# Performance work log

Hardware: AMD Instinct MI355X
Metric: run time of the kernel (lower is better)

## Reference

```python
import jax, jax.numpy as jnp
import numpy as np
from math import factorial, sqrt, pi

LMAX, NSH = 2, 9
F = 64
N_RBF = 20
N_INTER = 2
N_ATOMS = 1000
N_PAIRS = 10000
CUTOFF = 5.0

# ---------- Clebsch-Gordan coefficients for real spherical harmonics ----------

def _cg_complex(l1, m1, l2, m2, l3, m3):
    # <l1 m1 l2 m2 | l3 m3> via Racah formula
    if m3 != m1 + m2 or not (abs(l1 - l2) <= l3 <= l1 + l2):
        return 0.0
    f = factorial
    pre = sqrt((2 * l3 + 1) * f(l3 + l1 - l2) * f(l3 - l1 + l2) * f(l1 + l2 - l3) / f(l1 + l2 + l3 + 1))
    pre *= sqrt(f(l3 + m3) * f(l3 - m3) * f(l1 - m1) * f(l1 + m1) * f(l2 - m2) * f(l2 + m2))
    s = 0.0
    for k in range(l1 + l2 - l3 + 1):
        d = [k, l1 + l2 - l3 - k, l1 - m1 - k, l2 + m2 - k, l3 - l2 + m1 + k, l3 - l1 - m2 + k]
        if min(d) < 0:
            continue
        s += (-1) ** k / np.prod([float(f(t)) for t in d])
    return pre * s

def _sh_indices(lmax):
    l = np.concatenate([np.full(2 * ll + 1, ll) for ll in range(lmax + 1)])
    m = np.concatenate([np.arange(-ll, ll + 1) for ll in range(lmax + 1)])
    return l, m

def _real_cg(lmax):
    lidx, midx = _sh_indices(lmax)
    n = (lmax + 1) ** 2
    cgc = np.zeros((n, n, n))
    for a in range(n):
        for b in range(n):
            for c in range(n):
                cgc[a, b, c] = _cg_complex(lidx[a], midx[a], lidx[b], midx[b], lidx[c], midx[c])
    # complex -> real spherical harmonic change of basis (per degree l)
    U = np.zeros((n, n), dtype=np.complex128)
    for ll in range(lmax + 1):
        base = ll * ll + ll
        U[base, base] = 1.0
        for m in range(1, ll + 1):
            U[base + m, base - m] = 1 / sqrt(2)
            U[base + m, base + m] = (-1) ** m / sqrt(2)
            U[base - m, base - m] = 1j / sqrt(2)
            U[base - m, base + m] = -1j * (-1) ** m / sqrt(2)
    cgr = np.einsum('ijk,ai,bj,ck->abc', cgc.astype(np.complex128), U, U, U.conj())
    parity = (-1.0) ** lidx
    mask = (parity[:, None, None] * parity[None, :, None]) == parity[None, None, :]
    cgr = np.real(cgr) * mask
    cgr = np.transpose(cgr, (2, 0, 1))  # [s_out, s_in(x), s_filter(Y)]
    s1, s2, s3 = np.nonzero(np.abs(cgr) > 1e-9)
    return s1, s2, s3, cgr[s1, s2, s3].astype(np.float32), lidx

_S1, _S2, _S3, _CGV, _LIDX = _real_cg(LMAX)
IDX1 = jnp.asarray(_S1)            # output sh channel per CG path
IDX2 = jnp.asarray(_S2)            # input-feature sh channel per CG path
IDX3 = jnp.asarray(_S3)            # Ylm sh channel per CG path
CGVAL = jnp.asarray(_CGV)          # CG value per path
WIDX = jnp.asarray(_LIDX[_S3])     # radial-filter degree per CG path
LIDX = jnp.asarray(_LIDX)          # degree of each of the 9 sh channels

# ---------- real spherical harmonics (lmax=2, orthonormal, m=-l..l order) ----------

def _rsh(u):
    x, y, z = u[:, 0], u[:, 1], u[:, 2]
    c1 = sqrt(3.0 / (4.0 * pi))
    c2 = 0.5 * sqrt(15.0 / pi)
    return jnp.stack([
        jnp.full_like(x, 0.5 / sqrt(pi)),
        c1 * y, c1 * z, c1 * x,
        c2 * x * y,
        c2 * y * z,
        0.25 * sqrt(5.0 / pi) * (3.0 * z * z - 1.0),
        c2 * x * z,
        0.25 * sqrt(15.0 / pi) * (x * x - y * y),
    ], axis=1)


def setup_inputs() -> dict:
    key = jax.random.key(0)
    ks = jax.random.split(key, 10)
    atomic_numbers = jax.random.randint(ks[0], (N_ATOMS,), 0, 100)
    r_ij = 1.5 * jax.random.normal(ks[1], (N_PAIRS, 3), dtype=jnp.float32)
    idx_i = jnp.sort(jax.random.randint(ks[2], (N_PAIRS,), 0, N_ATOMS))
    idx_j = jax.random.randint(ks[3], (N_PAIRS,), 0, N_ATOMS)
    emb = jax.random.normal(ks[4], (100, F), dtype=jnp.float32)
    def s(k, sh, fan):
        return jax.random.normal(k, sh, dtype=jnp.float32) / float(np.sqrt(fan))
    Wf = s(ks[5], (N_INTER, N_RBF, (LMAX + 1) * F), N_RBF)
    bf = jnp.zeros((N_INTER, (LMAX + 1) * F), jnp.float32)
    W1 = s(ks[6], (N_INTER, F, F), F)
    W2 = s(ks[7], (N_INTER, F, F), F)
    W3 = s(ks[8], (N_INTER, F, F), F)
    Wg = s(ks[9], (N_INTER, F, (LMAX + 1) * F), F)
    bg = jnp.zeros((N_INTER, (LMAX + 1) * F), jnp.float32)
    return dict(atomic_numbers=atomic_numbers, r_ij=r_ij, idx_i=idx_i, idx_j=idx_j,
                emb=emb, Wf=Wf, bf=bf, W1=W1, W2=W2, W3=W3, Wg=Wg, bg=bg)


def reference(atomic_numbers, r_ij, idx_i, idx_j, emb, Wf, bf, W1, W2, W3, Wg, bg):
    n_atoms = atomic_numbers.shape[0]
    d = jnp.linalg.norm(r_ij, axis=1, keepdims=True)          # [P,1]
    Yij = _rsh(r_ij / d)                                       # [P,9]
    offsets = jnp.linspace(0.0, CUTOFF, N_RBF)                 # GaussianRBF
    width = CUTOFF / (N_RBF - 1)
    radial = jnp.exp((-0.5 / (width * width)) * (d - offsets) ** 2)   # [P,n_rbf]
    cut = 0.5 * (jnp.cos(d * (pi / CUTOFF)) + 1.0) * (d < CUTOFF)     # [P,1]
    # nuclear embedding + scalar2rsh (zero-pad l>0 channels)
    x = jnp.zeros((n_atoms, NSH, F), emb.dtype).at[:, 0, :].set(emb[atomic_numbers])
    for t in range(N_INTER):
        # SO3Convolution
        Wij = (radial @ Wf[t] + bf[t]).reshape(-1, LMAX + 1, F) * cut[:, :, None]  # [P,lmax+1,F]
        xj = x[idx_j]                                                              # [P,9,F]
        v = xj[:, IDX2] * Yij[:, IDX3, None] * Wij[:, WIDX] * CGVAL[None, :, None]  # [P,nnz,F]
        yij = jnp.zeros_like(xj).at[:, IDX1].add(v)                                 # CG scatter
        dx = jax.ops.segment_sum(yij, idx_i, num_segments=n_atoms)                  # edge->node scatter
        # mixing1 + SO3TensorProduct
        ddx = dx @ W1[t]
        tp = jnp.zeros_like(dx).at[:, IDX1].add(dx[:, IDX2] * ddx[:, IDX3] * CGVAL[None, :, None])
        dx = (dx + tp) @ W2[t]
        # SO3ParametricGatedNonlinearity (gate from l=0 channel)
        gate = (dx[:, 0] @ Wg[t] + bg[t]).reshape(-1, LMAX + 1, F)
        dx = dx * jax.nn.sigmoid(gate[:, LIDX])
        dx = dx @ W3[t]
        x = x + dx
    return x  # multipole_representation [n_atoms, 9, F]; x[:,0] is scalar_representation
```

## Files before the change

### kernel.cpp

```cpp
#include <hip/hip_runtime.h>
#include <cmath>

constexpr int kNsh    = 9;
constexpr int kF      = 64;
constexpr int kNrbf   = 20;
constexpr int kNAtoms = 1000;
constexpr int kNPairs = 10000;
constexpr float kCutoffF = 5.0f;
constexpr int kMaxNZ  = 200;
constexpr int kCp     = 12;
constexpr int kXs     = kF * kCp;
constexpr int kChunk  = 32;
constexpr int kPdS    = 36;

struct CGSparse {
  int n;
  int c[kMaxNZ];
  int a[kMaxNZ];
  int b[kMaxNZ];
  float v[kMaxNZ];
};

constexpr double cfact(int n) {
  double r = 1.0;
  for (int i = 2; i <= n; i++) r *= (double)i;
  return r;
}
constexpr double cabs_(double x) { return x < 0 ? -x : x; }
constexpr double csqrt_(double x) {
  if (x <= 0.0) return 0.0;
  double g = x < 1.0 ? 1.0 : x;
  for (int i = 0; i < 60; i++) g = 0.5 * (g + x / g);
  return g;
}

constexpr double cg_cplx(int l1, int m1, int l2, int m2, int l3, int m3) {
  if (m3 != m1 + m2) return 0.0;
  int lo = l1 > l2 ? l1 - l2 : l2 - l1;
  if (l3 < lo || l3 > l1 + l2) return 0.0;
  double pre = csqrt_((2 * l3 + 1) * cfact(l3 + l1 - l2) * cfact(l3 - l1 + l2) *
                      cfact(l1 + l2 - l3) / cfact(l1 + l2 + l3 + 1));
  pre *= csqrt_(cfact(l3 + m3) * cfact(l3 - m3) * cfact(l1 - m1) *
                cfact(l1 + m1) * cfact(l2 - m2) * cfact(l2 + m2));
  double s = 0.0;
  for (int k = 0; k <= l1 + l2 - l3; k++) {
    int d0 = k, d1 = l1 + l2 - l3 - k, d2 = l1 - m1 - k;
    int d3 = l2 + m2 - k, d4 = l3 - l2 + m1 + k, d5 = l3 - l1 - m2 + k;
    if (d0 < 0 || d1 < 0 || d2 < 0 || d3 < 0 || d4 < 0 || d5 < 0) continue;
    double den = cfact(d0) * cfact(d1) * cfact(d2) * cfact(d3) * cfact(d4) * cfact(d5);
    s += ((k % 2) ? -1.0 : 1.0) / den;
  }
  return pre * s;
}

constexpr CGSparse build_cg() {
  CGSparse out{};
  int lidx[9] = {0, 1, 1, 1, 2, 2, 2, 2, 2};
  int midx[9] = {0, -1, 0, 1, -2, -1, 0, 1, 2};
  double Ur[9][9] = {};
  double Ui[9][9] = {};
  for (int l = 0; l <= 2; l++) {
    int base = l * l + l;
    Ur[base][base] = 1.0;
    for (int m = 1; m <= l; m++) {
      double s2 = 1.0 / csqrt_(2.0);
      double sgn = (m % 2) ? -1.0 : 1.0;
      Ur[base + m][base - m] = s2;
      Ur[base + m][base + m] = sgn * s2;
      Ui[base - m][base - m] = s2;
      Ui[base - m][base + m] = -sgn * s2;
    }
  }
  double cgr[9][9][9] = {};
  for (int i = 0; i < 9; i++)
    for (int j = 0; j < 9; j++)
      for (int k = 0; k < 9; k++) {
        double cv = cg_cplx(lidx[i], midx[i], lidx[j], midx[j], lidx[k], midx[k]);
        if (cv == 0.0) continue;
        for (int a2 = 0; a2 < 9; a2++) {
          if (Ur[a2][i] == 0.0 && Ui[a2][i] == 0.0) continue;
          for (int b2 = 0; b2 < 9; b2++) {
            if (Ur[b2][j] == 0.0 && Ui[b2][j] == 0.0) continue;
            for (int c2 = 0; c2 < 9; c2++) {
              if (Ur[c2][k] == 0.0 && Ui[c2][k] == 0.0) continue;
              double ar = Ur[a2][i], ai = Ui[a2][i];
              double br = Ur[b2][j], bi = Ui[b2][j];
              double cr = Ur[c2][k], ci = -Ui[c2][k];
              double pr = ar * br - ai * bi;
              double pi = ar * bi + ai * br;
              double rr = pr * cr - pi * ci;
              cgr[c2][a2][b2] += rr * cv;
            }
          }
        }
      }
  int n = 0;
  for (int c2 = 0; c2 < 9; c2++)
    for (int a2 = 0; a2 < 9; a2++)
      for (int b2 = 0; b2 < 9; b2++) {
        bool mask = ((lidx[a2] + lidx[b2]) % 2) == (lidx[c2] % 2);
        double v = mask ? cgr[c2][a2][b2] : 0.0;
        if (cabs_(v) > 1e-9) {
          out.c[n] = c2;
          out.a[n] = a2;
          out.b[n] = b2;
          out.v[n] = (float)v;
          n++;
        }
      }
  out.n = n;
  return out;
}

constexpr CGSparse CG = build_cg();
static_assert(CG.n > 0 && CG.n <= kMaxNZ, "CG table size out of range");

__device__ __forceinline__ void mm_stream(const float* __restrict__ sDx,
                                          const float* __restrict__ W,
                                          int f, float* __restrict__ acc) {
  #pragma unroll
  for (int c = 0; c < 9; c++) acc[c] = 0.f;
  #pragma unroll 4
  for (int kq = 0; kq < 16; kq++) {
    float w0 = W[(4 * kq + 0) * kF + f];
    float w1 = W[(4 * kq + 1) * kF + f];
    float w2 = W[(4 * kq + 2) * kF + f];
    float w3 = W[(4 * kq + 3) * kF + f];
    #pragma unroll
    for (int c = 0; c < 9; c++) {
      float4 dv = *(const float4*)(sDx + c * kF + 4 * kq);
      acc[c] += dv.x * w0 + dv.y * w1 + dv.z * w2 + dv.w * w3;
    }
  }
}

template <int T>
__global__ __launch_bounds__(64) void k_so3(
    const float* __restrict__ rij, const int* __restrict__ idx_i,
    const int* __restrict__ idx_j, const int* __restrict__ Z,
    const float* __restrict__ emb, const float* __restrict__ Wft,
    const float* __restrict__ bft, const float* __restrict__ W1,
    const float* __restrict__ W2, const float* __restrict__ W3,
    const float* __restrict__ Wg, const float* __restrict__ bg,
    const float* __restrict__ x_in, float* __restrict__ x_out) {
  const int atom = blockIdx.x;
  const int f = threadIdx.x;

  __shared__ __align__(16) float pdLDS[kChunk * kPdS];
  __shared__ __align__(16) float dxLDS[kNsh * kF];
  __shared__ __align__(16) float rowLDS[kF];

  float w0r[kNrbf], w1r[kNrbf], w2r[kNrbf];
  #pragma unroll
  for (int k = 0; k < kNrbf; k++) {
    w0r[k] = Wft[k * 192 + f];
    w1r[k] = Wft[k * 192 + 64 + f];
    w2r[k] = Wft[k * 192 + 128 + f];
  }
  const float bf0 = bft[f], bf1 = bft[64 + f], bf2 = bft[128 + f];

  int lo = 0;
  {
    const int a = atom + (f & 1);
    int hi = kNPairs;
    while (lo < hi) {
      int mid = (lo + hi) >> 1;
      if (idx_i[mid] < a) lo = mid + 1; else hi = mid;
    }
  }
  const int s0 = __builtin_amdgcn_readlane(lo, 0);
  const int s1 = __builtin_amdgcn_readlane(lo, 1);

  float y[9];
  #pragma unroll
  for (int c = 0; c < 9; c++) y[c] = 0.f;

  for (int cb = s0; cb < s1; cb += kChunk) {
    const int cn = (s1 - cb < kChunk) ? (s1 - cb) : kChunk;
    for (int item = f; item < cn * 32; item += 64) {
      const int pp = item >> 5, slot = item & 31;
      const int p = cb + pp;
      float rx = rij[3 * p + 0], ry = rij[3 * p + 1], rz = rij[3 * p + 2];
      float d = sqrtf(rx * rx + ry * ry + rz * rz);
      float inv = 1.0f / d;
      float ux = rx * inv, uy = ry * inv, uz = rz * inv;
      const float c0 = 0.28209479177387814f;
      const float c1 = 0.4886025119029199f;
      const float c2 = 1.0925484305920792f;
      const float c3 = 0.31539156525252005f;
      const float c4 = 0.5462742152960396f;
      float cut = (d < kCutoffF) ? 0.5f * (cosf(d * (float)(M_PI / 5.0)) + 1.0f) : 0.0f;
      float val;
      if (slot < 9) {
        val =
            (slot == 0) ? c0 :
            (slot == 1) ? c1 * uy :
            (slot == 2) ? c1 * uz :
            (slot == 3) ? c1 * ux :
            (slot == 4) ? c2 * ux * uy :
            (slot == 5) ? c2 * uy * uz :
            (slot == 6) ? c3 * (3.0f * uz * uz - 1.0f) :
            (slot == 7) ? c2 * ux * uz :
                          c4 * (ux * ux - uy * uy);
      } else if (slot == 9) {
        val = cut;
      } else if (slot >= 12) {
        const float width = kCutoffF / (kNrbf - 1);
        const float coef = -0.5f / (width * width);
        float off = (kCutoffF * (slot - 12)) / (kNrbf - 1);
        float tt = d - off;
        val = expf(coef * tt * tt) * cut;
      } else {
        continue;
      }
      pdLDS[pp * kPdS + slot] = val;
    }
    __syncthreads();

    for (int pp = 0; pp < cn; pp++) {
      const int p = cb + pp;
      const int j = idx_j[p];
      const float* pd = pdLDS + pp * kPdS;
      const float cut = pd[9];
      float Wl0 = bf0 * cut, Wl1 = bf1 * cut, Wl2 = bf2 * cut;
      #pragma unroll
      for (int kq = 0; kq < 5; kq++) {
        float4 r4 = *(const float4*)(pd + 12 + 4 * kq);
        Wl0 += r4.x * w0r[4 * kq] + r4.y * w0r[4 * kq + 1] +
               r4.z * w0r[4 * kq + 2] + r4.w * w0r[4 * kq + 3];
        Wl1 += r4.x * w1r[4 * kq] + r4.y * w1r[4 * kq + 1] +
               r4.z * w1r[4 * kq + 2] + r4.w * w1r[4 * kq + 3];
        Wl2 += r4.x * w2r[4 * kq] + r4.y * w2r[4 * kq + 1] +
               r4.z * w2r[4 * kq + 2] + r4.w * w2r[4 * kq + 3];
      }
      float YW[9];
      YW[0] = pd[0] * Wl0;
      YW[1] = pd[1] * Wl1;
      YW[2] = pd[2] * Wl1;
      YW[3] = pd[3] * Wl1;
      #pragma unroll
      for (int b = 4; b < 9; b++) YW[b] = pd[b] * Wl2;
      if (T == 0) {
        float e = emb[Z[j] * kF + f];
        #pragma unroll
        for (int q = 0; q < CG.n; q++) {
          if (CG.a[q] == 0) y[CG.c[q]] += CG.v[q] * YW[CG.b[q]] * e;
        }
      } else {
        const float* xj = x_in + j * kXs + f * kCp;
        float xv[12];
        *(float4*)&xv[0] = *(const float4*)(xj + 0);
        *(float4*)&xv[4] = *(const float4*)(xj + 4);
        *(float4*)&xv[8] = *(const float4*)(xj + 8);
        #pragma unroll
        for (int q = 0; q < CG.n; q++) {
          y[CG.c[q]] += CG.v[q] * YW[CG.b[q]] * xv[CG.a[q]];
        }
      }
    }
    __syncthreads();
  }

  #pragma unroll
  for (int c = 0; c < 9; c++) dxLDS[c * kF + f] = y[c];
  __syncthreads();
  float ddx[9];
  mm_stream(dxLDS, W1, f, ddx);

  float t2[9];
  #pragma unroll
  for (int c = 0; c < 9; c++) t2[c] = y[c];
  #pragma unroll
  for (int q = 0; q < CG.n; q++) {
    t2[CG.c[q]] += CG.v[q] * y[CG.a[q]] * ddx[CG.b[q]];
  }

  __syncthreads();
  #pragma unroll
  for (int c = 0; c < 9; c++) dxLDS[c * kF + f] = t2[c];
  __syncthreads();
  float dx2[9];
  mm_stream(dxLDS, W2, f, dx2);

  rowLDS[f] = dx2[0];
  __syncthreads();
  float g0 = bg[f], g1 = bg[64 + f], g2 = bg[128 + f];
  #pragma unroll 4
  for (int kq = 0; kq < 16; kq++) {
    float4 a4 = *(const float4*)(rowLDS + 4 * kq);
    float av[4] = {a4.x, a4.y, a4.z, a4.w};
    #pragma unroll
    for (int qq = 0; qq < 4; qq++) {
      const int k = 4 * kq + qq;
      g0 += av[qq] * Wg[k * 192 + f];
      g1 += av[qq] * Wg[k * 192 + 64 + f];
      g2 += av[qq] * Wg[k * 192 + 128 + f];
    }
  }
  g0 = 1.f / (1.f + expf(-g0));
  g1 = 1.f / (1.f + expf(-g1));
  g2 = 1.f / (1.f + expf(-g2));

  float dx3[9];
  dx3[0] = dx2[0] * g0;
  dx3[1] = dx2[1] * g1;
  dx3[2] = dx2[2] * g1;
  dx3[3] = dx2[3] * g1;
  #pragma unroll
  for (int c = 4; c < 9; c++) dx3[c] = dx2[c] * g2;

  __syncthreads();
  #pragma unroll
  for (int c = 0; c < 9; c++) dxLDS[c * kF + f] = dx3[c];
  __syncthreads();
  float o[9];
  mm_stream(dxLDS, W3, f, o);

  if (T == 0) {
    float r0 = emb[Z[atom] * kF + f];
    float buf[12];
    #pragma unroll
    for (int c = 0; c < 9; c++) buf[c] = o[c];
    buf[0] += r0;
    buf[9] = 0.f; buf[10] = 0.f; buf[11] = 0.f;
    float* dst = x_out + atom * kXs + f * kCp;
    *(float4*)(dst + 0) = *(float4*)&buf[0];
    *(float4*)(dst + 4) = *(float4*)&buf[4];
    *(float4*)(dst + 8) = *(float4*)&buf[8];
  } else {
    const float* xi = x_in + atom * kXs + f * kCp;
    float xv[12];
    *(float4*)&xv[0] = *(const float4*)(xi + 0);
    *(float4*)&xv[4] = *(const float4*)(xi + 4);
    *(float4*)&xv[8] = *(const float4*)(xi + 8);
    #pragma unroll
    for (int c = 0; c < 9; c++) {
      x_out[atom * (kNsh * kF) + c * kF + f] = o[c] + xv[c];
    }
  }
}

extern "C" void kernel_launch(void* const* d_in, const int* in_sizes, int n_in,
                              void* d_out, int out_size, void* d_ws, size_t ws_size,
                              hipStream_t stream) {
  const int* Z        = (const int*)d_in[0];
  const float* rij    = (const float*)d_in[1];
  const int* idx_i    = (const int*)d_in[2];
  const int* idx_j    = (const int*)d_in[3];
  const float* emb    = (const float*)d_in[4];
  const float* Wf     = (const float*)d_in[5];
  const float* bf     = (const float*)d_in[6];
  const float* W1     = (const float*)d_in[7];
  const float* W2     = (const float*)d_in[8];
  const float* W3     = (const float*)d_in[9];
  const float* Wg     = (const float*)d_in[10];
  const float* bg     = (const float*)d_in[11];
  float* out = (float*)d_out;

  float* x1 = (float*)d_ws;

  k_so3<0><<<kNAtoms, 64, 0, stream>>>(
      rij, idx_i, idx_j, Z, emb, Wf, bf,
      W1, W2, W3, Wg, bg, (const float*)nullptr, x1);

  k_so3<1><<<kNAtoms, 64, 0, stream>>>(
      rij, idx_i, idx_j, Z, emb, Wf + kNrbf * 192, bf + 192,
      W1 + kF * kF, W2 + kF * kF, W3 + kF * kF,
      Wg + kF * 192, bg + 192, x1, out);
}
```

Baseline: 152.5 us.

## Split per-atom SO3 kernel into per-pair message kernel with atomics plus node update

Replaces the fused per-atom kernel, which loops serially over each atom's pairs, with a pair-parallel message kernel that computes filters, spherical harmonics and CG products per pair and scatters them into a zeroed per-atom buffer with atomicAdd. A separate per-atom kernel then performs the mixing, tensor product and gating. This aims to expose more parallelism and remove per-atom load imbalance and the binary search. The cost is a memset, twice as many launches, 90k atomics per layer and an extra global round trip for dx, and the summation order is no longer deterministic.

```diff
diff --git a/kernel.cpp b/kernel.cpp
--- a/kernel.cpp
+++ b/kernel.cpp
@@ -10,8 +10,7 @@
 constexpr int kMaxNZ  = 200;
 constexpr int kCp     = 12;
 constexpr int kXs     = kF * kCp;
-constexpr int kChunk  = 32;
-constexpr int kPdS    = 36;
+constexpr int kDx     = kNsh * kF;
 
 struct CGSparse {
   int n;
@@ -115,6 +114,95 @@
 constexpr CGSparse CG = build_cg();
 static_assert(CG.n > 0 && CG.n <= kMaxNZ, "CG table size out of range");
 
+template <int T>
+__global__ __launch_bounds__(256) void k_msg(
+    const float* __restrict__ rij, const int* __restrict__ idx_i,
+    const int* __restrict__ idx_j, const int* __restrict__ Z,
+    const float* __restrict__ emb, const float* __restrict__ Wft,
+    const float* __restrict__ bft, const float* __restrict__ x_in,
+    float* __restrict__ dxg) {
+  const int p = blockIdx.x * 4 + (threadIdx.x >> 6);
+  const int f = threadIdx.x & 63;
+
+  const float rx = rij[3 * p + 0], ry = rij[3 * p + 1], rz = rij[3 * p + 2];
+  const float d = sqrtf(rx * rx + ry * ry + rz * rz);
+  const float inv = 1.0f / d;
+  const float ux = rx * inv, uy = ry * inv, uz = rz * inv;
+  const float cut = (d < kCutoffF) ? 0.5f * (cosf(d * (float)(M_PI / 5.0)) + 1.0f) : 0.0f;
+
+  const float c0 = 0.28209479177387814f;
+  const float c1 = 0.4886025119029199f;
+  const float c2 = 1.0925484305920792f;
+  const float c3 = 0.31539156525252005f;
+  const float c4 = 0.5462742152960396f;
+  float Y[9];
+  Y[0] = c0;
+  Y[1] = c1 * uy;
+  Y[2] = c1 * uz;
+  Y[3] = c1 * ux;
+  Y[4] = c2 * ux * uy;
+  Y[5] = c2 * uy * uz;
+  Y[6] = c3 * (3.0f * uz * uz - 1.0f);
+  Y[7] = c2 * ux * uz;
+  Y[8] = c4 * (ux * ux - uy * uy);
+
+  const float width = kCutoffF / (kNrbf - 1);
+  const float coef = -0.5f / (width * width);
+  float rad[kNrbf];
+  #pragma unroll
+  for (int k = 0; k < kNrbf; k++) {
+    float off = (kCutoffF * k) / (kNrbf - 1);
+    float tt = d - off;
+    rad[k] = expf(coef * tt * tt) * cut;
+  }
+
+  float Wl0 = bft[f] * cut, Wl1 = bft[64 + f] * cut, Wl2 = bft[128 + f] * cut;
+  #pragma unroll 5
+  for (int k = 0; k < kNrbf; k++) {
+    Wl0 += rad[k] * Wft[k * 192 + f];
+    Wl1 += rad[k] * Wft[k * 192 + 64 + f];
+    Wl2 += rad[k] * Wft[k * 192 + 128 + f];
+  }
+
+  float YW[9];
+  YW[0] = Y[0] * Wl0;
+  YW[1] = Y[1] * Wl1;
+  YW[2] = Y[2] * Wl1;
+  YW[3] = Y[3] * Wl1;
+  #pragma unroll
+  for (int b = 4; b < 9; b++) YW[b] = Y[b] * Wl2;
+
+  const int i = idx_i[p];
+  const int j = idx_j[p];
+
+  float y[9];
+  #pragma unroll
+  for (int c = 0; c < 9; c++) y[c] = 0.f;
+  if (T == 0) {
+    float e = emb[Z[j] * kF + f];
+    #pragma unroll
+    for (int q = 0; q < CG.n; q++) {
+      if (CG.a[q] == 0) y[CG.c[q]] += CG.v[q] * YW[CG.b[q]] * e;
+    }
+  } else {
+    const float* xj = x_in + j * kXs + f * kCp;
+    float xv[12];
+    *(float4*)&xv[0] = *(const float4*)(xj + 0);
+    *(float4*)&xv[4] = *(const float4*)(xj + 4);
+    *(float4*)&xv[8] = *(const float4*)(xj + 8);
+    #pragma unroll
+    for (int q = 0; q < CG.n; q++) {
+      y[CG.c[q]] += CG.v[q] * YW[CG.b[q]] * xv[CG.a[q]];
+    }
+  }
+
+  float* dst = dxg + i * kDx + f;
+  #pragma unroll
+  for (int c = 0; c < 9; c++) {
+    atomicAdd(dst + c * kF, y[c]);
+  }
+}
+
 __device__ __forceinline__ void mm_stream(const float* __restrict__ sDx,
                                           const float* __restrict__ W,
                                           int f, float* __restrict__ acc) {
@@ -135,131 +223,21 @@
 }
 
 template <int T>
-__global__ __launch_bounds__(64) void k_so3(
-    const float* __restrict__ rij, const int* __restrict__ idx_i,
-    const int* __restrict__ idx_j, const int* __restrict__ Z,
-    const float* __restrict__ emb, const float* __restrict__ Wft,
-    const float* __restrict__ bft, const float* __restrict__ W1,
-    const float* __restrict__ W2, const float* __restrict__ W3,
-    const float* __restrict__ Wg, const float* __restrict__ bg,
+__global__ __launch_bounds__(64) void k_upd(
+    const int* __restrict__ Z, const float* __restrict__ emb,
+    const float* __restrict__ W1, const float* __restrict__ W2,
+    const float* __restrict__ W3, const float* __restrict__ Wg,
+    const float* __restrict__ bg, const float* __restrict__ dxg,
     const float* __restrict__ x_in, float* __restrict__ x_out) {
   const int atom = blockIdx.x;
   const int f = threadIdx.x;
 
-  __shared__ __align__(16) float pdLDS[kChunk * kPdS];
   __shared__ __align__(16) float dxLDS[kNsh * kF];
   __shared__ __align__(16) float rowLDS[kF];
 
-  float w0r[kNrbf], w1r[kNrbf], w2r[kNrbf];
-  #pragma unroll
-  for (int k = 0; k < kNrbf; k++) {
-    w0r[k] = Wft[k * 192 + f];
-    w1r[k] = Wft[k * 192 + 64 + f];
-    w2r[k] = Wft[k * 192 + 128 + f];
-  }
-  const float bf0 = bft[f], bf1 = bft[64 + f], bf2 = bft[128 + f];
-
-  int lo = 0;
-  {
-    const int a = atom + (f & 1);
-    int hi = kNPairs;
-    while (lo < hi) {
-      int mid = (lo + hi) >> 1;
-      if (idx_i[mid] < a) lo = mid + 1; else hi = mid;
-    }
-  }
-  const int s0 = __builtin_amdgcn_readlane(lo, 0);
-  const int s1 = __builtin_amdgcn_readlane(lo, 1);
-
   float y[9];
   #pragma unroll
-  for (int c = 0; c < 9; c++) y[c] = 0.f;
-
-  for (int cb = s0; cb < s1; cb += kChunk) {
-    const int cn = (s1 - cb < kChunk) ? (s1 - cb) : kChunk;
-    for (int item = f; item < cn * 32; item += 64) {
-      const int pp = item >> 5, slot = item & 31;
-      const int p = cb + pp;
-      float rx = rij[3 * p + 0], ry = rij[3 * p + 1], rz = rij[3 * p + 2];
-      float d = sqrtf(rx * rx + ry * ry + rz * rz);
-      float inv = 1.0f / d;
-      float ux = rx * inv, uy = ry * inv, uz = rz * inv;
-      const float c0 = 0.28209479177387814f;
-      const float c1 = 0.4886025119029199f;
-      const float c2 = 1.0925484305920792f;
-      const float c3 = 0.31539156525252005f;
-      const float c4 = 0.5462742152960396f;
-      float cut = (d < kCutoffF) ? 0.5f * (cosf(d * (float)(M_PI / 5.0)) + 1.0f) : 0.0f;
-      float val;
-      if (slot < 9) {
-        val =
-            (slot == 0) ? c0 :
-            (slot == 1) ? c1 * uy :
-            (slot == 2) ? c1 * uz :
-            (slot == 3) ? c1 * ux :
-            (slot == 4) ? c2 * ux * uy :
-            (slot == 5) ? c2 * uy * uz :
-            (slot == 6) ? c3 * (3.0f * uz * uz - 1.0f) :
-            (slot == 7) ? c2 * ux * uz :
-                          c4 * (ux * ux - uy * uy);
-      } else if (slot == 9) {
-        val = cut;
-      } else if (slot >= 12) {
-        const float width = kCutoffF / (kNrbf - 1);
-        const float coef = -0.5f / (width * width);
-        float off = (kCutoffF * (slot - 12)) / (kNrbf - 1);
-        float tt = d - off;
-        val = expf(coef * tt * tt) * cut;
-      } else {
-        continue;
-      }
-      pdLDS[pp * kPdS + slot] = val;
-    }
-    __syncthreads();
-
-    for (int pp = 0; pp < cn; pp++) {
-      const int p = cb + pp;
-      const int j = idx_j[p];
-      const float* pd = pdLDS + pp * kPdS;
-      const float cut = pd[9];
-      float Wl0 = bf0 * cut, Wl1 = bf1 * cut, Wl2 = bf2 * cut;
-      #pragma unroll
-      for (int kq = 0; kq < 5; kq++) {
-        float4 r4 = *(const float4*)(pd + 12 + 4 * kq);
-        Wl0 += r4.x * w0r[4 * kq] + r4.y * w0r[4 * kq + 1] +
-               r4.z * w0r[4 * kq + 2] + r4.w * w0r[4 * kq + 3];
-        Wl1 += r4.x * w1r[4 * kq] + r4.y * w1r[4 * kq + 1] +
-               r4.z * w1r[4 * kq + 2] + r4.w * w1r[4 * kq + 3];
-        Wl2 += r4.x * w2r[4 * kq] + r4.y * w2r[4 * kq + 1] +
-               r4.z * w2r[4 * kq + 2] + r4.w * w2r[4 * kq + 3];
-      }
-      float YW[9];
-      YW[0] = pd[0] * Wl0;
-      YW[1] = pd[1] * Wl1;
-      YW[2] = pd[2] * Wl1;
-      YW[3] = pd[3] * Wl1;
-      #pragma unroll
-      for (int b = 4; b < 9; b++) YW[b] = pd[b] * Wl2;
-      if (T == 0) {
-        float e = emb[Z[j] * kF + f];
-        #pragma unroll
-        for (int q = 0; q < CG.n; q++) {
-          if (CG.a[q] == 0) y[CG.c[q]] += CG.v[q] * YW[CG.b[q]] * e;
-        }
-      } else {
-        const float* xj = x_in + j * kXs + f * kCp;
-        float xv[12];
-        *(float4*)&xv[0] = *(const float4*)(xj + 0);
-        *(float4*)&xv[4] = *(const float4*)(xj + 4);
-        *(float4*)&xv[8] = *(const float4*)(xj + 8);
-        #pragma unroll
-        for (int q = 0; q < CG.n; q++) {
-          y[CG.c[q]] += CG.v[q] * YW[CG.b[q]] * xv[CG.a[q]];
-        }
-      }
-    }
-    __syncthreads();
-  }
+  for (int c = 0; c < 9; c++) y[c] = dxg[atom * kDx + c * kF + f];
 
   #pragma unroll
   for (int c = 0; c < 9; c++) dxLDS[c * kF + f] = y[c];
@@ -357,14 +335,20 @@
   const float* bg     = (const float*)d_in[11];
   float* out = (float*)d_out;
 
-  float* x1 = (float*)d_ws;
-
-  k_so3<0><<<kNAtoms, 64, 0, stream>>>(
-      rij, idx_i, idx_j, Z, emb, Wf, bf,
-      W1, W2, W3, Wg, bg, (const float*)nullptr, x1);
-
-  k_so3<1><<<kNAtoms, 64, 0, stream>>>(
-      rij, idx_i, idx_j, Z, emb, Wf + kNrbf * 192, bf + 192,
-      W1 + kF * kF, W2 + kF * kF, W3 + kF * kF,
-      Wg + kF * 192, bg + 192, x1, out);
-}
+  float* x1   = (float*)d_ws;
+  float* dxg0 = x1 + kNAtoms * kXs;
+  float* dxg1 = dxg0 + kNAtoms * kDx;
+
+  hipMemsetAsync(dxg0, 0, 2 * kNAtoms * kDx * sizeof(float), stream);
+
+  k_msg<0><<<kNPairs / 4, 256, 0, stream>>>(
+      rij, idx_i, idx_j, Z, emb, Wf, bf, (const float*)nullptr, dxg0);
+  k_upd<0><<<kNAtoms, 64, 0, stream>>>(
+      Z, emb, W1, W2, W3, Wg, bg, dxg0, (const float*)nullptr, x1);
+
+  k_msg<1><<<kNPairs / 4, 256, 0, stream>>>(
+      rij, idx_i, idx_j, Z, emb, Wf + kNrbf * 192, bf + 192, x1, dxg1);
+  k_upd<1><<<kNAtoms, 64, 0, stream>>>(
+      Z, emb, W1 + kF * kF, W2 + kF * kF, W3 + kF * kF,
+      Wg + kF * 192, bg + 192, dxg1, x1, out);
+}
```

Result: slower. 176.8 us (+15.9%).
